# Performance work log

Measured on AMD Instinct MI355X. Metric: run time of the kernel, lower is better.

Reference implementation:

```python
import jax, jax.numpy as jnp
import numpy as np

WINDOW = 2


def _fo_pool(h, f):
    """c_t = f_t * c_{t-1} + (1 - f_t) * h_t with c_{-1} = 0, scanned over axis 1 (time).
    Implemented as an associative scan on affine maps (a, b): c -> a*c + b."""
    def combine(left, right):
        a1, b1 = left
        a2, b2 = right
        return a2 * a1, a2 * b1 + b2
    a = f
    b = (1.0 - f) * h
    _, c = jax.lax.associative_scan(combine, (a, b), axis=1)
    return c


def setup_inputs() -> dict:
    key = jax.random.key(0)
    k1, k2 = jax.random.split(key)
    B, T, C, U = 8, 2048, 1024, 1024
    x = jax.random.normal(k1, (B, T, C), dtype=jnp.float32)
    # Keras Conv1D kernel layout: [window, in_channels, out_channels]; glorot-ish scale
    scale = (2.0 / (C + 3 * U)) ** 0.5
    kernel = jax.random.normal(k2, (WINDOW, C, 3 * U), dtype=jnp.float32) * scale
    bias = jnp.zeros((3 * U,), dtype=jnp.float32)
    return {"x": x, "kernel": kernel, "bias": bias}


def reference(x, kernel, bias):
    # causal conv1d: pad (window-1) on the left of time axis
    gv = jax.lax.conv_general_dilated(
        x, kernel,
        window_strides=(1,),
        padding=[(WINDOW - 1, 0)],
        dimension_numbers=("NWC", "WIO", "NWC"),
    ) + bias  # [B, T, 3U]
    hidden, forget, output = jnp.split(gv, 3, axis=-1)
    hidden = jnp.tanh(hidden)
    forget = jax.nn.sigmoid(forget)
    c = _fo_pool(hidden, forget)           # [B, T, U]
    h = jax.nn.sigmoid(output) * c          # output gate
    return h
```

## Files before the change

### kernel.cpp

```cpp
#include <hip/hip_runtime.h>


typedef _Float16 f16;
typedef _Float16 f16x8 __attribute__((ext_vector_type(8)));
typedef float    f32x4 __attribute__((ext_vector_type(4)));

#define Bq 8
#define Tq 2048
#define Cq 1024
#define Uq 1024
#define Mq (Bq*Tq)
#define Kq (2*Cq)
#define Nq (3*Uq)
#define NCH 32
#define CHL (Tq/NCH)

#define AS1 __attribute__((address_space(1)))
#define AS3 __attribute__((address_space(3)))

__global__ void prep_xs(const float* __restrict__ x, f16* __restrict__ Xs) {
    long long idx = ((long long)blockIdx.x * blockDim.x + threadIdx.x) * 8;
    int c = (int)(idx & (Cq - 1));
    long long row = idx >> 10;
    int tp = (int)(row % (Tq + 1));
    int b  = (int)(row / (Tq + 1));
    f16x8 o;
    if (tp == 0) {
#pragma unroll
        for (int j = 0; j < 8; j++) o[j] = (f16)0.0f;
    } else {
        const float* src = x + (((size_t)b * Tq + (tp - 1)) << 10) + c;
        float4 v0 = *(const float4*)(src);
        float4 v1 = *(const float4*)(src + 4);
        o[0]=(f16)v0.x; o[1]=(f16)v0.y; o[2]=(f16)v0.z; o[3]=(f16)v0.w;
        o[4]=(f16)v1.x; o[5]=(f16)v1.y; o[6]=(f16)v1.z; o[7]=(f16)v1.w;
    }
    *(f16x8*)(Xs + idx) = o;
}

__global__ void prep_wt(const float* __restrict__ w, f16* __restrict__ WT) {
    __shared__ float t[32][33];
    int kb = blockIdx.x * 32, nb = blockIdx.y * 32;
    int tx = threadIdx.x & 31, ty = threadIdx.x >> 5;
#pragma unroll
    for (int j = 0; j < 32; j += 8)
        t[ty + j][tx] = w[(size_t)(kb + ty + j) * Nq + nb + tx];
    __syncthreads();
#pragma unroll
    for (int j = 0; j < 32; j += 8)
        WT[(size_t)(nb + ty + j) * Kq + kb + tx] = (f16)t[tx][ty + j];
}

__global__ __launch_bounds__(512, 2) void gemm_gates8(
    const f16* __restrict__ Xs, const f16* __restrict__ WT,
    const float* __restrict__ bias,
    f16* __restrict__ H, f16* __restrict__ F, f16* __restrict__ O)
{
    __shared__ __align__(16) f16 smem[65536];
    const int tid  = threadIdx.x;
    const int lane = tid & 63;
    const int wave = tid >> 6;
    const int wm = wave >> 2;
    const int wn = wave & 3;

    const int wg  = blockIdx.x;
    const int swz = (wg & 7) * 96 + (wg >> 3);
    const int mT  = swz / 12, nT = swz - mT * 12;
    const int rM  = mT * 256;
    const int nB  = nT * 256;
    const int b   = rM >> 11;
    const int t0  = rM & (Tq - 1);
    const size_t xsRow0 = (size_t)b * (Tq + 1) + t0;

    const int srow = tid >> 3;
    const int scol = (((tid & 7) ^ (srow & 7))) * 8;
    const f16* Abase = Xs + (xsRow0 + srow) * (size_t)Cq + scol;
    const f16* Bbase = WT + (size_t)(nB + srow) * Kq + scol;
    const int dstT = tid * 16;

#define STAGE_A(c, h, kt) do { \
    const f16* _s = Abase + (size_t)((h) * 128) * Cq + (kt) * 64; \
    int _d = (c) * 65536 + (h) * 16384 + dstT; \
    __builtin_amdgcn_global_load_lds((const AS1 void*)_s, \
        (AS3 void*)((char*)smem + _d), 16, 0, 0); \
    __builtin_amdgcn_global_load_lds((const AS1 void*)(_s + (size_t)64 * Cq), \
        (AS3 void*)((char*)smem + _d + 8192), 16, 0, 0); \
} while (0)

#define STAGE_B(c, h, kt) do { \
    const f16* _s = Bbase + (size_t)((h) * 128) * Kq + (kt) * 64; \
    int _d = 32768 + (c) * 65536 + (h) * 16384 + dstT; \
    __builtin_amdgcn_global_load_lds((const AS1 void*)_s, \
        (AS3 void*)((char*)smem + _d), 16, 0, 0); \
    __builtin_amdgcn_global_load_lds((const AS1 void*)(_s + (size_t)64 * Kq), \
        (AS3 void*)((char*)smem + _d + 8192), 16, 0, 0); \
} while (0)

    const int rAoff = (wm * 64 + (lane & 15)) * 128;
    const int rBoff = (wn * 32 + (lane & 15)) * 128;
    const int ksw0 = (((lane >> 4) * 16)) ^ ((lane & 7) << 4);
    const int ksw1 = (64 + ((lane >> 4) * 16)) ^ ((lane & 7) << 4);

    f32x4 acc[2][2][4][2] = {};
    f16x8 afA[4][2], afB[4][2], bg0[2][2], bg1[2][2];

#define LOADA_TO(c, h, dst) do { \
    const char* _a = (const char*)smem + (c) * 65536 + (h) * 16384 + rAoff; \
    _Pragma("unroll") \
    for (int mi = 0; mi < 4; mi++) { \
        dst[mi][0] = *(const f16x8*)(_a + mi * 2048 + ksw0); \
        dst[mi][1] = *(const f16x8*)(_a + mi * 2048 + ksw1); \
    } \
} while (0)

#define LOADB_TO(c, g, breg) do { \
    const char* _b = (const char*)smem + 32768 + (c) * 65536 + (g) * 16384 + rBoff; \
    _Pragma("unroll") \
    for (int ni = 0; ni < 2; ni++) { \
        breg[ni][0] = *(const f16x8*)(_b + ni * 2048 + ksw0); \
        breg[ni][1] = *(const f16x8*)(_b + ni * 2048 + ksw1); \
    } \
} while (0)

#define MM(h, g, afr, breg) do { \
    _Pragma("unroll") \
    for (int mi = 0; mi < 4; mi++) \
    _Pragma("unroll") \
    for (int ni = 0; ni < 2; ni++) { \
        acc[h][g][mi][ni] = __builtin_amdgcn_mfma_f32_16x16x32_f16(afr[mi][0], breg[ni][0], acc[h][g][mi][ni], 0, 0, 0); \
        acc[h][g][mi][ni] = __builtin_amdgcn_mfma_f32_16x16x32_f16(afr[mi][1], breg[ni][1], acc[h][g][mi][ni], 0, 0, 0); \
    } \
} while (0)

#define BAR()  __builtin_amdgcn_s_barrier()
#define SB0()  __builtin_amdgcn_sched_barrier(0)
#define PRIO1  __builtin_amdgcn_s_setprio(1)
#define PRIO0  __builtin_amdgcn_s_setprio(0)
#define LGKMC(n) asm volatile("s_waitcnt lgkmcnt(" #n ")" ::: "memory")
#define VM2()    asm volatile("s_waitcnt vmcnt(2)" ::: "memory")

#define KTILE(c, ktn) do { \
     LOADB_TO(c, 1, bg1); STAGE_A(1 - (c), 0, ktn); \
           SB0(); LGKMC(4); SB0(); \
           PRIO1; MM(0, 0, afA, bg0); PRIO0; \
           VM2(); BAR(); \
     LOADA_TO(c, 1, afB); STAGE_B(1 - (c), 0, ktn); \
           SB0(); LGKMC(8); SB0(); \
           PRIO1; MM(0, 1, afA, bg1); PRIO0; \
     STAGE_B(1 - (c), 1, ktn); \
           SB0(); LGKMC(0); SB0(); \
           PRIO1; MM(1, 0, afB, bg0); PRIO0; \
           VM2(); BAR(); \
     LOADA_TO(1 - (c), 0, afA); LOADB_TO(1 - (c), 0, bg0); STAGE_A(1 - (c), 1, ktn); \
           SB0(); LGKMC(12); SB0(); \
           PRIO1; MM(1, 1, afB, bg1); PRIO0; \
           VM2(); BAR(); \
} while (0)

    STAGE_A(0, 0, 0); STAGE_B(0, 0, 0); STAGE_B(0, 1, 0); STAGE_A(0, 1, 0);
    asm volatile("s_waitcnt vmcnt(2)" ::: "memory");
    BAR();
    LOADA_TO(0, 0, afA); LOADB_TO(0, 0, bg0);

    for (int t = 0; t < 32; t += 2) {
        KTILE(0, t + 1);
        KTILE(1, t + 2);
    }

    const int gate = nB >> 10;
    f16* G = (gate == 0) ? H : ((gate == 1) ? F : O);
#pragma unroll
    for (int h = 0; h < 2; h++)
#pragma unroll
    for (int g = 0; g < 2; g++)
#pragma unroll
    for (int ni = 0; ni < 2; ni++) {
        const int col = nB + g * 128 + wn * 32 + ni * 16 + (lane & 15);
        const int u = col & (Uq - 1);
        const float bv = bias[col];
#pragma unroll
        for (int mi = 0; mi < 4; mi++)
#pragma unroll
        for (int j = 0; j < 4; j++) {
            const int row = rM + h * 128 + wm * 64 + mi * 16 + ((lane >> 4) << 2) + j;
            float v = acc[h][g][mi][ni][j] + bv;
            float r;
            if (gate == 0) r = 1.0f - 2.0f / (__expf(2.0f * v) + 1.0f);
            else           r = 1.0f / (1.0f + __expf(-v));
            G[(size_t)row * Uq + u] = (f16)r;
        }
    }
}

__global__ void scan_pass1(const f16* __restrict__ F, const f16* __restrict__ H,
                           float* __restrict__ Ach, float* __restrict__ Bch) {
    int idx = blockIdx.x * blockDim.x + threadIdx.x;
    int u  = idx & (Uq - 1);
    int ch = (idx >> 10) & (NCH - 1);
    int b  = idx >> 15;
    size_t base = ((size_t)b * Tq + ch * CHL) * Uq + u;
    float a = 1.0f, c = 0.0f;
    for (int i = 0; i < CHL; i++) {
        float f = (float)F[base + (size_t)i * Uq];
        float h = (float)H[base + (size_t)i * Uq];
        c = f * c + (1.0f - f) * h;
        a *= f;
    }
    Ach[idx] = a;
    Bch[idx] = c;
}

__global__ void scan_pass2(const float* __restrict__ Ach, const float* __restrict__ Bch,
                           float* __restrict__ Cin) {
    int idx = blockIdx.x * blockDim.x + threadIdx.x;
    int u = idx & (Uq - 1);
    int b = idx >> 10;
    float c = 0.0f;
    for (int ch = 0; ch < NCH; ch++) {
        int o = ((b * NCH) + ch) * Uq + u;
        Cin[o] = c;
        c = Ach[o] * c + Bch[o];
    }
}

__global__ void scan_pass3(const f16* __restrict__ F, const f16* __restrict__ H,
                           const f16* __restrict__ O, const float* __restrict__ Cin,
                           float* __restrict__ out) {
    int idx = blockIdx.x * blockDim.x + threadIdx.x;
    int u  = idx & (Uq - 1);
    int ch = (idx >> 10) & (NCH - 1);
    int b  = idx >> 15;
    size_t base = ((size_t)b * Tq + ch * CHL) * Uq + u;
    float c = Cin[idx];
    for (int i = 0; i < CHL; i++) {
        float f = (float)F[base + (size_t)i * Uq];
        float h = (float)H[base + (size_t)i * Uq];
        c = f * c + (1.0f - f) * h;
        out[base + (size_t)i * Uq] = (float)O[base + (size_t)i * Uq] * c;
    }
}

extern "C" void kernel_launch(void* const* d_in, const int* in_sizes, int n_in,
                              void* d_out, int out_size, void* d_ws, size_t ws_size,
                              hipStream_t stream) {
    const float* x    = (const float*)d_in[0];
    const float* w    = (const float*)d_in[1];
    const float* bias = (const float*)d_in[2];
    float* out = (float*)d_out;
    char* ws = (char*)d_ws;

    f16* Xs   = (f16*)(ws);
    f16* WT   = (f16*)(ws + 33570816);
    f16* Hh   = (f16*)(ws + 46153728);
    f16* Fh   = (f16*)(ws + 79708160);
    f16* Oh   = (f16*)(ws + 113262592);
    float* Ach = (float*)(ws + 146817024);
    float* Bch = (float*)(ws + 147865600);
    float* Cin = (float*)(ws + 148914176);

    prep_xs<<<(Bq * (Tq + 1) * Cq) / (8 * 256), 256, 0, stream>>>(x, Xs);
    prep_wt<<<dim3(Kq / 32, Nq / 32), 256, 0, stream>>>(w, WT);
    gemm_gates8<<<(Mq / 256) * (Nq / 256), 512, 0, stream>>>(Xs, WT, bias, Hh, Fh, Oh);
    scan_pass1<<<(Bq * NCH * Uq) / 256, 256, 0, stream>>>(Fh, Hh, Ach, Bch);
    scan_pass2<<<(Bq * Uq) / 256, 256, 0, stream>>>(Ach, Bch, Cin);
    scan_pass3<<<(Bq * NCH * Uq) / 256, 256, 0, stream>>>(Fh, Hh, Oh, Cin, out);
}
```

Baseline: 256.6 us.

## Merge prep kernels, drop scan pass2, and vectorize scan passes by two

Result: faster. 251.2 us (-2.1%).

```diff
diff --git a/kernel.cpp b/kernel.cpp
--- a/kernel.cpp
+++ b/kernel.cpp
@@ -2,6 +2,7 @@
 
 
 typedef _Float16 f16;
+typedef _Float16 f16x2 __attribute__((ext_vector_type(2)));
 typedef _Float16 f16x8 __attribute__((ext_vector_type(8)));
 typedef float    f32x4 __attribute__((ext_vector_type(4)));
 
@@ -14,41 +15,45 @@
 #define Nq (3*Uq)
 #define NCH 32
 #define CHL (Tq/NCH)
+#define NXBLK 8196
 
 #define AS1 __attribute__((address_space(1)))
 #define AS3 __attribute__((address_space(3)))
 
-__global__ void prep_xs(const float* __restrict__ x, f16* __restrict__ Xs) {
-    long long idx = ((long long)blockIdx.x * blockDim.x + threadIdx.x) * 8;
-    int c = (int)(idx & (Cq - 1));
-    long long row = idx >> 10;
-    int tp = (int)(row % (Tq + 1));
-    int b  = (int)(row / (Tq + 1));
-    f16x8 o;
-    if (tp == 0) {
-#pragma unroll
-        for (int j = 0; j < 8; j++) o[j] = (f16)0.0f;
+__global__ void prep_all(const float* __restrict__ x, const float* __restrict__ w,
+                         f16* __restrict__ Xs, f16* __restrict__ WT) {
+    __shared__ float t[32][33];
+    if (blockIdx.x < NXBLK) {
+        long long idx = ((long long)blockIdx.x * blockDim.x + threadIdx.x) * 8;
+        int c = (int)(idx & (Cq - 1));
+        long long row = idx >> 10;
+        int tp = (int)(row % (Tq + 1));
+        int b  = (int)(row / (Tq + 1));
+        f16x8 o;
+        if (tp == 0) {
+#pragma unroll
+            for (int j = 0; j < 8; j++) o[j] = (f16)0.0f;
+        } else {
+            const float* src = x + (((size_t)b * Tq + (tp - 1)) << 10) + c;
+            float4 v0 = *(const float4*)(src);
+            float4 v1 = *(const float4*)(src + 4);
+            o[0]=(f16)v0.x; o[1]=(f16)v0.y; o[2]=(f16)v0.z; o[3]=(f16)v0.w;
+            o[4]=(f16)v1.x; o[5]=(f16)v1.y; o[6]=(f16)v1.z; o[7]=(f16)v1.w;
+        }
+        *(f16x8*)(Xs + idx) = o;
     } else {
-        const float* src = x + (((size_t)b * Tq + (tp - 1)) << 10) + c;
-        float4 v0 = *(const float4*)(src);
-        float4 v1 = *(const float4*)(src + 4);
-        o[0]=(f16)v0.x; o[1]=(f16)v0.y; o[2]=(f16)v0.z; o[3]=(f16)v0.w;
-        o[4]=(f16)v1.x; o[5]=(f16)v1.y; o[6]=(f16)v1.z; o[7]=(f16)v1.w;
-    }
-    *(f16x8*)(Xs + idx) = o;
-}
-
-__global__ void prep_wt(const float* __restrict__ w, f16* __restrict__ WT) {
-    __shared__ float t[32][33];
-    int kb = blockIdx.x * 32, nb = blockIdx.y * 32;
-    int tx = threadIdx.x & 31, ty = threadIdx.x >> 5;
-#pragma unroll
-    for (int j = 0; j < 32; j += 8)
-        t[ty + j][tx] = w[(size_t)(kb + ty + j) * Nq + nb + tx];
-    __syncthreads();
-#pragma unroll
-    for (int j = 0; j < 32; j += 8)
-        WT[(size_t)(nb + ty + j) * Kq + kb + tx] = (f16)t[tx][ty + j];
+        int wtid = blockIdx.x - NXBLK;
+        int kb = (wtid & 63) * 32;
+        int nb = (wtid >> 6) * 32;
+        int tx = threadIdx.x & 31, ty = threadIdx.x >> 5;
+#pragma unroll
+        for (int j = 0; j < 32; j += 8)
+            t[ty + j][tx] = w[(size_t)(kb + ty + j) * Nq + nb + tx];
+        __syncthreads();
+#pragma unroll
+        for (int j = 0; j < 32; j += 8)
+            WT[(size_t)(nb + ty + j) * Kq + kb + tx] = (f16)t[tx][ty + j];
+    }
 }
 
 __global__ __launch_bounds__(512, 2) void gemm_gates8(
@@ -195,48 +200,51 @@
 __global__ void scan_pass1(const f16* __restrict__ F, const f16* __restrict__ H,
                            float* __restrict__ Ach, float* __restrict__ Bch) {
     int idx = blockIdx.x * blockDim.x + threadIdx.x;
-    int u  = idx & (Uq - 1);
-    int ch = (idx >> 10) & (NCH - 1);
-    int b  = idx >> 15;
+    int u  = (idx & 511) * 2;
+    int ch = (idx >> 9) & (NCH - 1);
+    int b  = idx >> 14;
     size_t base = ((size_t)b * Tq + ch * CHL) * Uq + u;
-    float a = 1.0f, c = 0.0f;
+    float a0 = 1.0f, a1 = 1.0f, c0 = 0.0f, c1 = 0.0f;
     for (int i = 0; i < CHL; i++) {
-        float f = (float)F[base + (size_t)i * Uq];
-        float h = (float)H[base + (size_t)i * Uq];
-        c = f * c + (1.0f - f) * h;
-        a *= f;
-    }
-    Ach[idx] = a;
-    Bch[idx] = c;
-}
-
-__global__ void scan_pass2(const float* __restrict__ Ach, const float* __restrict__ Bch,
-                           float* __restrict__ Cin) {
-    int idx = blockIdx.x * blockDim.x + threadIdx.x;
-    int u = idx & (Uq - 1);
-    int b = idx >> 10;
-    float c = 0.0f;
-    for (int ch = 0; ch < NCH; ch++) {
-        int o = ((b * NCH) + ch) * Uq + u;
-        Cin[o] = c;
-        c = Ach[o] * c + Bch[o];
-    }
+        f16x2 fv = *(const f16x2*)(F + base + (size_t)i * Uq);
+        f16x2 hv = *(const f16x2*)(H + base + (size_t)i * Uq);
+        float f0 = (float)fv[0], f1 = (float)fv[1];
+        c0 = f0 * c0 + (1.0f - f0) * (float)hv[0];
+        c1 = f1 * c1 + (1.0f - f1) * (float)hv[1];
+        a0 *= f0; a1 *= f1;
+    }
+    int o = ((b * NCH + ch) << 10) + u;
+    *(float2*)(Ach + o) = make_float2(a0, a1);
+    *(float2*)(Bch + o) = make_float2(c0, c1);
 }
 
 __global__ void scan_pass3(const f16* __restrict__ F, const f16* __restrict__ H,
-                           const f16* __restrict__ O, const float* __restrict__ Cin,
+                           const f16* __restrict__ O,
+                           const float* __restrict__ Ach, const float* __restrict__ Bch,
                            float* __restrict__ out) {
     int idx = blockIdx.x * blockDim.x + threadIdx.x;
-    int u  = idx & (Uq - 1);
-    int ch = (idx >> 10) & (NCH - 1);
-    int b  = idx >> 15;
+    int u  = (idx & 511) * 2;
+    int ch = (idx >> 9) & (NCH - 1);
+    int b  = idx >> 14;
+    int cbase = (b * NCH << 10) + u;
+    float c0 = 0.0f, c1 = 0.0f;
+    for (int ch2 = 0; ch2 < ch; ch2++) {
+        int o = cbase + (ch2 << 10);
+        float2 av = *(const float2*)(Ach + o);
+        float2 bv = *(const float2*)(Bch + o);
+        c0 = av.x * c0 + bv.x;
+        c1 = av.y * c1 + bv.y;
+    }
     size_t base = ((size_t)b * Tq + ch * CHL) * Uq + u;
-    float c = Cin[idx];
     for (int i = 0; i < CHL; i++) {
-        float f = (float)F[base + (size_t)i * Uq];
-        float h = (float)H[base + (size_t)i * Uq];
-        c = f * c + (1.0f - f) * h;
-        out[base + (size_t)i * Uq] = (float)O[base + (size_t)i * Uq] * c;
+        f16x2 fv = *(const f16x2*)(F + base + (size_t)i * Uq);
+        f16x2 hv = *(const f16x2*)(H + base + (size_t)i * Uq);
+        f16x2 ov = *(const f16x2*)(O + base + (size_t)i * Uq);
+        float f0 = (float)fv[0], f1 = (float)fv[1];
+        c0 = f0 * c0 + (1.0f - f0) * (float)hv[0];
+        c1 = f1 * c1 + (1.0f - f1) * (float)hv[1];
+        *(float2*)(out + base + (size_t)i * Uq) =
+            make_float2((float)ov[0] * c0, (float)ov[1] * c1);
     }
 }
 
@@ -256,12 +264,9 @@
     f16* Oh   = (f16*)(ws + 113262592);
     float* Ach = (float*)(ws + 146817024);
     float* Bch = (float*)(ws + 147865600);
-    float* Cin = (float*)(ws + 148914176);
-
-    prep_xs<<<(Bq * (Tq + 1) * Cq) / (8 * 256), 256, 0, stream>>>(x, Xs);
-    prep_wt<<<dim3(Kq / 32, Nq / 32), 256, 0, stream>>>(w, WT);
+
+    prep_all<<<NXBLK + 6144, 256, 0, stream>>>(x, w, Xs, WT);
     gemm_gates8<<<(Mq / 256) * (Nq / 256), 512, 0, stream>>>(Xs, WT, bias, Hh, Fh, Oh);
-    scan_pass1<<<(Bq * NCH * Uq) / 256, 256, 0, stream>>>(Fh, Hh, Ach, Bch);
-    scan_pass2<<<(Bq * Uq) / 256, 256, 0, stream>>>(Ach, Bch, Cin);
-    scan_pass3<<<(Bq * NCH * Uq) / 256, 256, 0, stream>>>(Fh, Hh, Oh, Cin, out);
-}
+    scan_pass1<<<(Bq * NCH * (Uq / 2)) / 256, 256, 0, stream>>>(Fh, Hh, Ach, Bch);
+    scan_pass3<<<(Bq * NCH * (Uq / 2)) / 256, 256, 0, stream>>>(Fh, Hh, Oh, Ach, Bch, out);
+}
```
